# Performance work log

Hardware: AMD Instinct MI355X
Metric: run time of the kernel (lower is better)

The kernel has to match this reference:

```python
import jax, jax.numpy as jnp
import numpy as np

U, I, N, E, F, H, TOPK = 2048, 16384, 18432, 1_000_000, 64, 32, 3
NEG = -1e30  # stands in for 'structural zero' entries excluded from top-k


def setup_inputs() -> dict:
    key = jax.random.key(0)
    ks = jax.random.split(key, 6)
    x = jax.random.normal(ks[0], (N, F), dtype=jnp.float32)
    w1 = jax.random.normal(ks[1], (H, 2 * F + 2), dtype=jnp.float32) * 0.1
    b1 = jnp.zeros((H,), dtype=jnp.float32)
    w2 = jax.random.normal(ks[2], (1, H), dtype=jnp.float32) * 0.1
    b2 = jnp.zeros((1,), dtype=jnp.float32)
    edge_src = jax.random.randint(ks[3], (E,), 0, U)        # user-local == global (user_idx = arange)
    edge_dst_item = jax.random.randint(ks[4], (E,), 0, I)   # item-local; global item id = U + item
    user_idx = jnp.arange(U, dtype=jnp.int64) if jax.config.jax_enable_x64 else jnp.arange(U, dtype=jnp.int32)
    return {"x": x, "w1": w1, "b1": b1, "w2": w2, "b2": b2,
            "edge_src": edge_src, "edge_dst_item": edge_dst_item,
            "user_idx": user_idx, "num_nodes": N}


def reference(x, w1, b1, w2, b2, edge_src, edge_dst_item, user_idx, num_nodes):
    num_users = user_idx.shape[0]
    num_items = num_nodes - num_users
    u_local = edge_src           # user_idx = arange(U) so user_map is identity
    i_local = edge_dst_item      # item nodes occupy indices [U, N)

    ones = jnp.ones(u_local.shape[0], dtype=jnp.float32)
    d_u = jnp.log1p(jax.ops.segment_sum(ones, u_local, num_segments=num_users))  # [U]
    d_i = jnp.log1p(jax.ops.segment_sum(ones, i_local, num_segments=num_items))  # [I]

    # per-edge features: [u_x, log1p(deg_u), i_x, log1p(deg_i)] -> [E, 2F+2]
    x_u = x[user_idx[u_local]]
    x_it = x[num_users + i_local]
    x_e = jnp.concatenate([x_u, d_u[u_local][:, None], x_it, d_i[i_local][:, None]], axis=1)
    h = jax.nn.relu(x_e @ w1.T + b1)
    w = jax.nn.sigmoid(h @ w2.T + b2)[:, 0]  # [E], edge weights in (0,1)

    # A' [U, I] (duplicate edges coalesce-summed), C = A' A'^T with degree scaling
    A = jnp.zeros((num_users, num_items), dtype=jnp.float32).at[u_local, i_local].add(w)
    C = A @ A.T
    Dh = jnp.sqrt(d_u)
    C = C * Dh[:, None] * Dh[None, :]

    # per-row top-k restricted to structural nonzeros (all weights > 0)
    Cm = jnp.where(C > 0, C, NEG)
    vals, idx = jax.lax.top_k(Cm, TOPK)          # [U, K]
    valid = vals > 0
    vhalf = jnp.where(valid, vals, 0.0) * 0.5
    rows = jnp.broadcast_to(jnp.arange(num_users)[:, None], (num_users, TOPK))
    T = jnp.zeros((num_users, num_users), dtype=jnp.float32).at[rows, idx].add(vhalf)
    S = T + T.T  # symmetrized, deduped-by-sum adjacency; S[r,c] = val of edge (r,c)
    return S, d_u
```

## Files before the change

### kernel.cpp

```cpp
#include <hip/hip_runtime.h>
#include <hip/hip_bf16.h>
#include <math.h>

#define U_N 2048
#define I_N 16384
#define F_N 64
#define H_N 32
#define KDIM 16384
#define NEGV (-1e30f)
#define NB_DEG 256

typedef __attribute__((ext_vector_type(8))) short short8;
typedef __attribute__((ext_vector_type(4))) float f32x4;

__device__ __forceinline__ unsigned short f2bf(float f) {
    unsigned int u = __builtin_bit_cast(unsigned int, f);
    return (unsigned short)((u + 0x7fffu + ((u >> 16) & 1u)) >> 16);
}

__device__ __forceinline__ void gload16(const void* g, void* l) {
    __builtin_amdgcn_global_load_lds(
        (const __attribute__((address_space(1))) unsigned int*)g,
        (__attribute__((address_space(3))) unsigned int*)l, 16, 0, 0);
}

__global__ __launch_bounds__(256) void k_deg_part(const int* __restrict__ src,
                                                  const int* __restrict__ dst, int E,
                                                  unsigned int* __restrict__ pu,
                                                  unsigned int* __restrict__ pi2) {
    __shared__ unsigned int hu[U_N];
    __shared__ unsigned int hi2[I_N / 2];
    int tid = threadIdx.x;
    for (int t = tid; t < U_N; t += 256) hu[t] = 0u;
    for (int t = tid; t < I_N / 2; t += 256) hi2[t] = 0u;
    __syncthreads();
    const int4* s4 = (const int4*)src;
    const int4* d4 = (const int4*)dst;
    int nv = E >> 2;
    for (int v = blockIdx.x * 256 + tid; v < nv; v += NB_DEG * 256) {
        int4 u = s4[v], i = d4[v];
        atomicAdd(&hu[u.x], 1u); atomicAdd(&hi2[i.x >> 1], 1u << ((i.x & 1) * 16));
        atomicAdd(&hu[u.y], 1u); atomicAdd(&hi2[i.y >> 1], 1u << ((i.y & 1) * 16));
        atomicAdd(&hu[u.z], 1u); atomicAdd(&hi2[i.z >> 1], 1u << ((i.z & 1) * 16));
        atomicAdd(&hu[u.w], 1u); atomicAdd(&hi2[i.w >> 1], 1u << ((i.w & 1) * 16));
    }
    if (blockIdx.x == 0) {
        int e = nv * 4 + tid;
        if (e < E) {
            atomicAdd(&hu[src[e]], 1u);
            int i = dst[e];
            atomicAdd(&hi2[i >> 1], 1u << ((i & 1) * 16));
        }
    }
    __syncthreads();
    unsigned int* pub = pu + (size_t)blockIdx.x * U_N;
    unsigned int* pib = pi2 + (size_t)blockIdx.x * (I_N / 2);
    for (int t = tid; t < U_N; t += 256) pub[t] = hu[t];
    for (int t = tid; t < I_N / 2; t += 256) pib[t] = hi2[t];
}

__global__ __launch_bounds__(256) void k_node(const unsigned int* __restrict__ pu,
                                              const unsigned int* __restrict__ pi2,
                                              float* __restrict__ du,
                                              float* __restrict__ di,
                                              float* __restrict__ Dh,
                                              float* __restrict__ out_du,
                                              unsigned int* __restrict__ degu) {
    int t = blockIdx.x * 256 + threadIdx.x;
    if (t < U_N) {
        unsigned int s = 0;
        for (int b = 0; b < NB_DEG; ++b) s += pu[(size_t)b * U_N + t];
        degu[t] = s;
        float v = log1pf((float)s);
        du[t] = v;
        Dh[t] = sqrtf(v);
        out_du[t] = v;
    }
    if (t < I_N / 2) {
        unsigned int s = 0;
        for (int b = 0; b < NB_DEG; ++b) s += pi2[(size_t)b * (I_N / 2) + t];
        di[2 * t]     = log1pf((float)(s & 0xffffu));
        di[2 * t + 1] = log1pf((float)(s >> 16));
    }
}

__global__ __launch_bounds__(64) void k_scan2(const unsigned int* __restrict__ pu,
                                              const unsigned int* __restrict__ degu,
                                              unsigned int* __restrict__ base,
                                              unsigned int* __restrict__ pof) {
    __shared__ unsigned int s[U_N];
    __shared__ unsigned int csum[64];
    int tid = threadIdx.x;
    for (int t = tid; t < U_N; t += 64) s[t] = degu[t];
    __syncthreads();
    unsigned int sum = 0;
#pragma unroll
    for (int j = 0; j < 32; ++j) sum += s[tid * 32 + j];
    csum[tid] = sum;
    __syncthreads();
    if (tid == 0) {
        unsigned int run = 0;
        for (int c = 0; c < 64; ++c) { unsigned int v = csum[c]; csum[c] = run; run += v; }
    }
    __syncthreads();
    {
        unsigned int run = csum[tid];
        unsigned int ex[32];
#pragma unroll
        for (int j = 0; j < 32; ++j) { ex[j] = run; run += s[tid * 32 + j]; }
        __syncthreads();
#pragma unroll
        for (int j = 0; j < 32; ++j) s[tid * 32 + j] = ex[j];
        __syncthreads();
    }
    int u = blockIdx.x * 64 + tid;
    unsigned int run = s[u];
    base[u] = run;
    for (int b = 0; b < NB_DEG; ++b) {
        pof[(size_t)b * U_N + u] = run;
        run += pu[(size_t)b * U_N + u];
    }
}

__global__ __launch_bounds__(256) void k_esort(const int* __restrict__ src,
                                               const int* __restrict__ dst, int E,
                                               const unsigned int* __restrict__ pof,
                                               unsigned short* __restrict__ sorted) {
    __shared__ unsigned int cur[U_N];
    int tid = threadIdx.x;
    const unsigned int* p = pof + (size_t)blockIdx.x * U_N;
    for (int t = tid; t < U_N; t += 256) cur[t] = p[t];
    __syncthreads();
    const int4* s4 = (const int4*)src;
    const int4* d4 = (const int4*)dst;
    int nv = E >> 2;
    for (int v = blockIdx.x * 256 + tid; v < nv; v += NB_DEG * 256) {
        int4 u = s4[v], i = d4[v];
        sorted[atomicAdd(&cur[u.x], 1u)] = (unsigned short)i.x;
        sorted[atomicAdd(&cur[u.y], 1u)] = (unsigned short)i.y;
        sorted[atomicAdd(&cur[u.z], 1u)] = (unsigned short)i.z;
        sorted[atomicAdd(&cur[u.w], 1u)] = (unsigned short)i.w;
    }
    if (blockIdx.x == 0) {
        int e = nv * 4 + tid;
        if (e < E)
            sorted[atomicAdd(&cur[src[e]], 1u)] = (unsigned short)dst[e];
    }
}

__global__ __launch_bounds__(256) void k_proj(const float* __restrict__ x,
                                              const float* __restrict__ w1,
                                              const float* __restrict__ b1,
                                              const float* __restrict__ du,
                                              const float* __restrict__ di,
                                              float* __restrict__ Pu,
                                              float* __restrict__ Pi) {
    int t = blockIdx.x * 256 + threadIdx.x;
    if (t < U_N * H_N) {
        int u = t >> 5, j = t & 31;
        const float* xr = x + (size_t)u * F_N;
        const float* wr = w1 + (size_t)j * (2 * F_N + 2);
        float acc = b1[j] + du[u] * wr[64];
#pragma unroll
        for (int f = 0; f < F_N; ++f) acc = fmaf(xr[f], wr[f], acc);
        Pu[t] = acc;
    } else if (t < U_N * H_N + I_N * H_N) {
        int t2 = t - U_N * H_N;
        int i = t2 >> 5, j = t2 & 31;
        const float* xr = x + (size_t)(U_N + i) * F_N;
        const float* wr = w1 + (size_t)j * (2 * F_N + 2) + 65;
        float acc = di[i] * wr[64];
#pragma unroll
        for (int f = 0; f < F_N; ++f) acc = fmaf(xr[f], wr[f], acc);
        Pi[t2] = acc;
    }
}

__global__ __launch_bounds__(256) void k_edge2(const unsigned short* __restrict__ sorted,
                                               const unsigned int* __restrict__ base,
                                               const unsigned int* __restrict__ degu,
                                               const float* __restrict__ Pu,
                                               const float* __restrict__ Pi,
                                               const float* __restrict__ w2,
                                               const float* __restrict__ b2,
                                               uint4* __restrict__ Aw,
                                               float* __restrict__ diag) {
    __shared__ float hrow[I_N];
    __shared__ float red[256];
    int u = blockIdx.x, tid = threadIdx.x;
    float4* h4 = (float4*)hrow;
    float4 z4 = {0.f, 0.f, 0.f, 0.f};
#pragma unroll
    for (int j = 0; j < 16; ++j) h4[tid + j * 256] = z4;

    float pur[H_N], w2r[H_N];
#pragma unroll
    for (int j = 0; j < H_N; ++j) pur[j] = Pu[(size_t)u * H_N + j];
#pragma unroll
    for (int j = 0; j < H_N; ++j) w2r[j] = w2[j];
    float bb = b2[0];
    __syncthreads();

    int nb = (int)base[u], d = (int)degu[u];
    for (int k = tid; k < d; k += 256) {
        int i = (int)sorted[nb + k];
        const float4* pi4 = (const float4*)(Pi + (size_t)i * H_N);
        float acc = bb;
#pragma unroll
        for (int q = 0; q < H_N / 4; ++q) {
            float4 b = pi4[q];
            acc = fmaf(fmaxf(pur[4 * q + 0] + b.x, 0.f), w2r[4 * q + 0], acc);
            acc = fmaf(fmaxf(pur[4 * q + 1] + b.y, 0.f), w2r[4 * q + 1], acc);
            acc = fmaf(fmaxf(pur[4 * q + 2] + b.z, 0.f), w2r[4 * q + 2], acc);
            acc = fmaf(fmaxf(pur[4 * q + 3] + b.w, 0.f), w2r[4 * q + 3], acc);
        }
        float wgt = 1.0f / (1.0f + expf(-acc));
        atomicAdd(&hrow[i], wgt);
    }
    __syncthreads();

    uint4* row = Aw + (size_t)u * (I_N / 8);
    float ss = 0.f;
#pragma unroll
    for (int j = 0; j < 8; ++j) {
        int w = tid + j * 256;
        float4 a = h4[2 * w], b = h4[2 * w + 1];
        uint4 o;
        o.x = (unsigned int)f2bf(a.x) | ((unsigned int)f2bf(a.y) << 16);
        o.y = (unsigned int)f2bf(a.z) | ((unsigned int)f2bf(a.w) << 16);
        o.z = (unsigned int)f2bf(b.x) | ((unsigned int)f2bf(b.y) << 16);
        o.w = (unsigned int)f2bf(b.z) | ((unsigned int)f2bf(b.w) << 16);
        row[w] = o;
        ss = fmaf(a.x, a.x, ss); ss = fmaf(a.y, a.y, ss);
        ss = fmaf(a.z, a.z, ss); ss = fmaf(a.w, a.w, ss);
        ss = fmaf(b.x, b.x, ss); ss = fmaf(b.y, b.y, ss);
        ss = fmaf(b.z, b.z, ss); ss = fmaf(b.w, b.w, ss);
    }
    red[tid] = ss;
    __syncthreads();
#pragma unroll
    for (int s = 128; s > 0; s >>= 1) {
        if (tid < s) red[tid] += red[tid + s];
        __syncthreads();
    }
    if (tid == 0) diag[u] = red[0];
}

#define BM 128
#define BKS 64
#define NBLK (U_N / BM)
#define NPAIR (NBLK * (NBLK + 1) / 2)
#define KSPLIT 4
#define KCH (KDIM / KSPLIT)

__global__ __launch_bounds__(256) void k_syrk(const unsigned short* __restrict__ Abf,
                                              float* __restrict__ C) {
    __shared__ unsigned short As[BM * BKS];
    __shared__ unsigned short Bs[BM * BKS];

    int k0 = blockIdx.x * KCH;
    int p = blockIdx.y;
    int bi = 0, rem = p;
    while (rem >= NBLK - bi) { rem -= NBLK - bi; ++bi; }
    int bj = bi + rem;
    int diagp = (bi == bj);

    int tid = threadIdx.x;
    int wave = tid >> 6, lane = tid & 63;

    int srow = wave * 32 + (lane >> 3);
    int scol = ((lane & 7) ^ (lane >> 3)) * 8;
    const unsigned short* Ag = Abf + (size_t)(bi * BM + srow) * KDIM + k0 + scol;
    const unsigned short* Bg = Abf + (size_t)(bj * BM + srow) * KDIM + k0 + scol;
    unsigned short* lA = As + (wave * 32) * BKS;
    unsigned short* lB = Bs + (wave * 32) * BKS;

    int wm = wave >> 1, wn = wave & 1;
    int lm = lane & 15, lq = lane >> 4;
    int lm7 = lm & 7;
    const unsigned short* bTile = diagp ? As : Bs;

    f32x4 acc[4][4];
#pragma unroll
    for (int m = 0; m < 4; ++m)
#pragma unroll
        for (int n = 0; n < 4; ++n) acc[m][n] = (f32x4){0.f, 0.f, 0.f, 0.f};

    for (int kt = 0; kt < KCH; kt += BKS) {
        __syncthreads();
#pragma unroll
        for (int j = 0; j < 4; ++j)
            gload16(Ag + kt + (size_t)(j * 8) * KDIM, lA + j * 8 * BKS);
        if (!diagp) {
#pragma unroll
            for (int j = 0; j < 4; ++j)
                gload16(Bg + kt + (size_t)(j * 8) * KDIM, lB + j * 8 * BKS);
        }
        __syncthreads();

#pragma unroll
        for (int s = 0; s < 2; ++s) {
            int pos = ((lq + s * 4) ^ lm7) * 8;
            short8 av[4], bv[4];
#pragma unroll
            for (int m = 0; m < 4; ++m)
                av[m] = *(const short8*)(As + (wm * 64 + m * 16 + lm) * BKS + pos);
#pragma unroll
            for (int n = 0; n < 4; ++n)
                bv[n] = *(const short8*)(bTile + (wn * 64 + n * 16 + lm) * BKS + pos);
#pragma unroll
            for (int m = 0; m < 4; ++m)
#pragma unroll
                for (int n = 0; n < 4; ++n)
                    acc[m][n] = __builtin_amdgcn_mfma_f32_16x16x32_bf16(
                        av[m], bv[n], acc[m][n], 0, 0, 0);
        }
    }

#pragma unroll
    for (int m = 0; m < 4; ++m) {
        int rb = bi * BM + wm * 64 + m * 16 + lq * 4;
#pragma unroll
        for (int n = 0; n < 4; ++n) {
            int c = bj * BM + wn * 64 + n * 16 + lm;
            f32x4 v = acc[m][n];
#pragma unroll
            for (int g = 0; g < 4; ++g)
                atomicAdd(&C[(size_t)(rb + g) * U_N + c], v[g]);
        }
    }
}

__global__ __launch_bounds__(256) void k_mirror(float* __restrict__ C) {
    __shared__ float T[64][65];
    int tr = blockIdx.x, tc = blockIdx.y;
    if ((tr >> 1) <= (tc >> 1)) return;
    int lane = threadIdx.x & 63;
    int w = threadIdx.x >> 6;
#pragma unroll
    for (int s = 0; s < 16; ++s) {
        int r = s * 4 + w;
        T[r][lane] = C[(size_t)(tc * 64 + r) * U_N + tr * 64 + lane];
    }
    __syncthreads();
#pragma unroll
    for (int s = 0; s < 16; ++s) {
        int r = s * 4 + w;
        C[(size_t)(tr * 64 + r) * U_N + tc * 64 + lane] = T[lane][r];
    }
}

__device__ __forceinline__ bool better(float va, int ia, float vb, int ib) {
    return (va > vb) || (va == vb && ia < ib);
}
__device__ __forceinline__ void ins3(float v, int i, float& v0, int& i0,
                                     float& v1, int& i1, float& v2, int& i2) {
    if (better(v, i, v0, i0)) { v2 = v1; i2 = i1; v1 = v0; i1 = i0; v0 = v; i0 = i; }
    else if (better(v, i, v1, i1)) { v2 = v1; i2 = i1; v1 = v; i1 = i; }
    else if (better(v, i, v2, i2)) { v2 = v; i2 = i; }
}

__global__ __launch_bounds__(256) void k_topk(const float* __restrict__ C,
                                              const float* __restrict__ Dh,
                                              const float* __restrict__ diag,
                                              float* __restrict__ out) {
    int wave = threadIdx.x >> 6, lane = threadIdx.x & 63;
    int r = blockIdx.x * 4 + wave;
    float dr = Dh[r];
    float dex = diag[r] * dr * dr;
    float dval = (dex > 0.f) ? dex : NEGV;
    const float4* row = (const float4*)(C + (size_t)r * U_N);
    const float4* dh4 = (const float4*)Dh;
    float v0 = NEGV, v1 = NEGV, v2 = NEGV;
    int i0 = 0x7fffffff, i1 = 0x7fffffff, i2 = 0x7fffffff;
    int qr = r >> 2;
    for (int q = lane; q < U_N / 4; q += 64) {
        float4 cv = row[q];
        float4 dv = dh4[q];
        int c = q * 4;
        float x0 = (cv.x > 0.f) ? cv.x * dr * dv.x : NEGV;
        float x1 = (cv.y > 0.f) ? cv.y * dr * dv.y : NEGV;
        float x2 = (cv.z > 0.f) ? cv.z * dr * dv.z : NEGV;
        float x3 = (cv.w > 0.f) ? cv.w * dr * dv.w : NEGV;
        if (q == qr) {
            int j = r & 3;
            if (j == 0) x0 = dval; else if (j == 1) x1 = dval;
            else if (j == 2) x2 = dval; else x3 = dval;
        }
        if (better(x0, c + 0, v2, i2)) ins3(x0, c + 0, v0, i0, v1, i1, v2, i2);
        if (better(x1, c + 1, v2, i2)) ins3(x1, c + 1, v0, i0, v1, i1, v2, i2);
        if (better(x2, c + 2, v2, i2)) ins3(x2, c + 2, v0, i0, v1, i1, v2, i2);
        if (better(x3, c + 3, v2, i2)) ins3(x3, c + 3, v0, i0, v1, i1, v2, i2);
    }
#pragma unroll
    for (int off = 1; off < 64; off <<= 1) {
        float ov0 = __shfl_xor(v0, off), ov1 = __shfl_xor(v1, off), ov2 = __shfl_xor(v2, off);
        int oi0 = __shfl_xor(i0, off), oi1 = __shfl_xor(i1, off), oi2 = __shfl_xor(i2, off);
        ins3(ov0, oi0, v0, i0, v1, i1, v2, i2);
        ins3(ov1, oi1, v0, i0, v1, i1, v2, i2);
        ins3(ov2, oi2, v0, i0, v1, i1, v2, i2);
    }
    if (lane == 0) {
        float vs[3] = {v0, v1, v2};
        int is[3] = {i0, i1, i2};
#pragma unroll
        for (int k = 0; k < 3; ++k) {
            if (vs[k] > 0.f) {
                atomicAdd(&out[(size_t)r * U_N + is[k]], 0.5f * vs[k]);
                atomicAdd(&out[(size_t)is[k] * U_N + r], 0.5f * vs[k]);
            }
        }
    }
}

extern "C" void kernel_launch(void* const* d_in, const int* in_sizes, int n_in,
                              void* d_out, int out_size, void* d_ws, size_t ws_size,
                              hipStream_t stream) {
    const float* x  = (const float*)d_in[0];
    const float* w1 = (const float*)d_in[1];
    const float* b1 = (const float*)d_in[2];
    const float* w2 = (const float*)d_in[3];
    const float* b2 = (const float*)d_in[4];
    const int* esrc = (const int*)d_in[5];
    const int* edst = (const int*)d_in[6];
    int E = in_sizes[5];
    float* out = (float*)d_out;

    unsigned short* Abf = (unsigned short*)d_ws;
    float* C    = (float*)(Abf + (size_t)U_N * I_N);
    float* Pu   = C + (size_t)U_N * U_N;
    float* Pi   = Pu + (size_t)U_N * H_N;
    unsigned int* pu  = (unsigned int*)(Pi + (size_t)I_N * H_N);
    unsigned int* pi2 = pu + (size_t)NB_DEG * U_N;
    unsigned int* pof = pi2 + (size_t)NB_DEG * (I_N / 2);
    unsigned int* degu = pof + (size_t)NB_DEG * U_N;
    unsigned int* base = degu + U_N;
    float* du   = (float*)(base + U_N);
    float* di   = du + U_N;
    float* Dh   = di + I_N;
    float* diag = Dh + U_N;
    unsigned short* sorted = (unsigned short*)(diag + U_N);

    hipMemsetAsync(C, 0, (size_t)U_N * U_N * sizeof(float), stream);
    hipMemsetAsync(out, 0, (size_t)out_size * sizeof(float), stream);

    k_deg_part<<<NB_DEG, 256, 0, stream>>>(esrc, edst, E, pu, pi2);
    k_node<<<(I_N / 2 + 255) / 256, 256, 0, stream>>>(pu, pi2, du, di, Dh,
                                                      out + (size_t)U_N * U_N, degu);
    k_scan2<<<U_N / 64, 64, 0, stream>>>(pu, degu, base, pof);
    k_proj<<<(U_N * H_N + I_N * H_N) / 256, 256, 0, stream>>>(x, w1, b1, du, di, Pu, Pi);
    k_esort<<<NB_DEG, 256, 0, stream>>>(esrc, edst, E, pof, sorted);
    k_edge2<<<U_N, 256, 0, stream>>>(sorted, base, degu, Pu, Pi, w2, b2,
                                     (uint4*)Abf, diag);
    k_syrk<<<dim3(KSPLIT, NPAIR), 256, 0, stream>>>(Abf, C);
    k_mirror<<<dim3(U_N / 64, U_N / 64), 256, 0, stream>>>(C);
    k_topk<<<U_N / 4, 256, 0, stream>>>(C, Dh, diag, out);
}
```

Measured before the change: 334.5 us.

## Fuse front-end kernels into one persistent kernel with software grid barriers

```diff
diff --git a/kernel.cpp b/kernel.cpp
--- a/kernel.cpp
+++ b/kernel.cpp
@@ -8,7 +8,7 @@
 #define H_N 32
 #define KDIM 16384
 #define NEGV (-1e30f)
-#define NB_DEG 256
+#define NB 256
 
 typedef __attribute__((ext_vector_type(8))) short short8;
 typedef __attribute__((ext_vector_type(4))) float f32x4;
@@ -24,226 +24,235 @@
         (__attribute__((address_space(3))) unsigned int*)l, 16, 0, 0);
 }
 
-__global__ __launch_bounds__(256) void k_deg_part(const int* __restrict__ src,
-                                                  const int* __restrict__ dst, int E,
-                                                  unsigned int* __restrict__ pu,
-                                                  unsigned int* __restrict__ pi2) {
-    __shared__ unsigned int hu[U_N];
-    __shared__ unsigned int hi2[I_N / 2];
-    int tid = threadIdx.x;
-    for (int t = tid; t < U_N; t += 256) hu[t] = 0u;
-    for (int t = tid; t < I_N / 2; t += 256) hi2[t] = 0u;
+__device__ __forceinline__ void gridbar(unsigned int* cnt, unsigned int k) {
     __syncthreads();
-    const int4* s4 = (const int4*)src;
-    const int4* d4 = (const int4*)dst;
-    int nv = E >> 2;
-    for (int v = blockIdx.x * 256 + tid; v < nv; v += NB_DEG * 256) {
-        int4 u = s4[v], i = d4[v];
-        atomicAdd(&hu[u.x], 1u); atomicAdd(&hi2[i.x >> 1], 1u << ((i.x & 1) * 16));
-        atomicAdd(&hu[u.y], 1u); atomicAdd(&hi2[i.y >> 1], 1u << ((i.y & 1) * 16));
-        atomicAdd(&hu[u.z], 1u); atomicAdd(&hi2[i.z >> 1], 1u << ((i.z & 1) * 16));
-        atomicAdd(&hu[u.w], 1u); atomicAdd(&hi2[i.w >> 1], 1u << ((i.w & 1) * 16));
-    }
-    if (blockIdx.x == 0) {
-        int e = nv * 4 + tid;
-        if (e < E) {
-            atomicAdd(&hu[src[e]], 1u);
-            int i = dst[e];
-            atomicAdd(&hi2[i >> 1], 1u << ((i & 1) * 16));
-        }
+    if (threadIdx.x == 0) {
+        __threadfence();
+        atomicAdd(cnt, 1u);
+        while (__hip_atomic_load(cnt, __ATOMIC_RELAXED, __HIP_MEMORY_SCOPE_AGENT)
+               < k * NB)
+            __builtin_amdgcn_s_sleep(8);
+        __threadfence();
     }
     __syncthreads();
-    unsigned int* pub = pu + (size_t)blockIdx.x * U_N;
-    unsigned int* pib = pi2 + (size_t)blockIdx.x * (I_N / 2);
-    for (int t = tid; t < U_N; t += 256) pub[t] = hu[t];
-    for (int t = tid; t < I_N / 2; t += 256) pib[t] = hi2[t];
-}
-
-__global__ __launch_bounds__(256) void k_node(const unsigned int* __restrict__ pu,
-                                              const unsigned int* __restrict__ pi2,
-                                              float* __restrict__ du,
-                                              float* __restrict__ di,
-                                              float* __restrict__ Dh,
-                                              float* __restrict__ out_du,
-                                              unsigned int* __restrict__ degu) {
-    int t = blockIdx.x * 256 + threadIdx.x;
-    if (t < U_N) {
-        unsigned int s = 0;
-        for (int b = 0; b < NB_DEG; ++b) s += pu[(size_t)b * U_N + t];
-        degu[t] = s;
-        float v = log1pf((float)s);
-        du[t] = v;
-        Dh[t] = sqrtf(v);
-        out_du[t] = v;
-    }
-    if (t < I_N / 2) {
-        unsigned int s = 0;
-        for (int b = 0; b < NB_DEG; ++b) s += pi2[(size_t)b * (I_N / 2) + t];
-        di[2 * t]     = log1pf((float)(s & 0xffffu));
-        di[2 * t + 1] = log1pf((float)(s >> 16));
-    }
-}
-
-__global__ __launch_bounds__(64) void k_scan2(const unsigned int* __restrict__ pu,
-                                              const unsigned int* __restrict__ degu,
-                                              unsigned int* __restrict__ base,
-                                              unsigned int* __restrict__ pof) {
-    __shared__ unsigned int s[U_N];
-    __shared__ unsigned int csum[64];
-    int tid = threadIdx.x;
-    for (int t = tid; t < U_N; t += 64) s[t] = degu[t];
-    __syncthreads();
-    unsigned int sum = 0;
-#pragma unroll
-    for (int j = 0; j < 32; ++j) sum += s[tid * 32 + j];
-    csum[tid] = sum;
-    __syncthreads();
-    if (tid == 0) {
-        unsigned int run = 0;
-        for (int c = 0; c < 64; ++c) { unsigned int v = csum[c]; csum[c] = run; run += v; }
-    }
+}
+
+__global__ __launch_bounds__(256) void k_front(
+        const int* __restrict__ src, const int* __restrict__ dst, int E,
+        const float* __restrict__ x, const float* __restrict__ w1,
+        const float* __restrict__ b1, const float* __restrict__ w2,
+        const float* __restrict__ b2,
+        unsigned int* __restrict__ pu, unsigned int* __restrict__ pi2,
+        unsigned int* __restrict__ base, unsigned int* __restrict__ pof,
+        unsigned int* __restrict__ degu,
+        float* __restrict__ du, float* __restrict__ di, float* __restrict__ Dh,
+        float* __restrict__ diag, float* __restrict__ Pu, float* __restrict__ Pi,
+        unsigned short* __restrict__ sorted, uint4* __restrict__ Aw,
+        float* __restrict__ C, float* __restrict__ out,
+        unsigned int* __restrict__ bar) {
+    __shared__ union {
+        struct { unsigned int hu[U_N]; unsigned int hi2[I_N / 2]; } h;
+        struct { unsigned int s[U_N]; unsigned int csum[256]; } sc;
+        unsigned int cur[U_N];
+        struct { float hrow[I_N]; float red[4]; } e;
+    } sm;
+
+    int bid = blockIdx.x, tid = threadIdx.x;
+    const float4 z4 = {0.f, 0.f, 0.f, 0.f};
+
+    for (int t = tid; t < U_N; t += 256) sm.h.hu[t] = 0u;
+    for (int t = tid; t < I_N / 2; t += 256) sm.h.hi2[t] = 0u;
     __syncthreads();
     {
-        unsigned int run = csum[tid];
-        unsigned int ex[32];
-#pragma unroll
-        for (int j = 0; j < 32; ++j) { ex[j] = run; run += s[tid * 32 + j]; }
-        __syncthreads();
-#pragma unroll
-        for (int j = 0; j < 32; ++j) s[tid * 32 + j] = ex[j];
-        __syncthreads();
-    }
-    int u = blockIdx.x * 64 + tid;
-    unsigned int run = s[u];
-    base[u] = run;
-    for (int b = 0; b < NB_DEG; ++b) {
-        pof[(size_t)b * U_N + u] = run;
-        run += pu[(size_t)b * U_N + u];
-    }
-}
-
-__global__ __launch_bounds__(256) void k_esort(const int* __restrict__ src,
-                                               const int* __restrict__ dst, int E,
-                                               const unsigned int* __restrict__ pof,
-                                               unsigned short* __restrict__ sorted) {
-    __shared__ unsigned int cur[U_N];
-    int tid = threadIdx.x;
-    const unsigned int* p = pof + (size_t)blockIdx.x * U_N;
-    for (int t = tid; t < U_N; t += 256) cur[t] = p[t];
+        const int4* s4 = (const int4*)src;
+        const int4* d4 = (const int4*)dst;
+        int nv = E >> 2;
+        for (int v = bid * 256 + tid; v < nv; v += NB * 256) {
+            int4 u = s4[v], i = d4[v];
+            atomicAdd(&sm.h.hu[u.x], 1u); atomicAdd(&sm.h.hi2[i.x >> 1], 1u << ((i.x & 1) * 16));
+            atomicAdd(&sm.h.hu[u.y], 1u); atomicAdd(&sm.h.hi2[i.y >> 1], 1u << ((i.y & 1) * 16));
+            atomicAdd(&sm.h.hu[u.z], 1u); atomicAdd(&sm.h.hi2[i.z >> 1], 1u << ((i.z & 1) * 16));
+            atomicAdd(&sm.h.hu[u.w], 1u); atomicAdd(&sm.h.hi2[i.w >> 1], 1u << ((i.w & 1) * 16));
+        }
+        if (bid == 0) {
+            int e = nv * 4 + tid;
+            if (e < E) {
+                atomicAdd(&sm.h.hu[src[e]], 1u);
+                int i = dst[e];
+                atomicAdd(&sm.h.hi2[i >> 1], 1u << ((i & 1) * 16));
+            }
+        }
+    }
     __syncthreads();
-    const int4* s4 = (const int4*)src;
-    const int4* d4 = (const int4*)dst;
-    int nv = E >> 2;
-    for (int v = blockIdx.x * 256 + tid; v < nv; v += NB_DEG * 256) {
-        int4 u = s4[v], i = d4[v];
-        sorted[atomicAdd(&cur[u.x], 1u)] = (unsigned short)i.x;
-        sorted[atomicAdd(&cur[u.y], 1u)] = (unsigned short)i.y;
-        sorted[atomicAdd(&cur[u.z], 1u)] = (unsigned short)i.z;
-        sorted[atomicAdd(&cur[u.w], 1u)] = (unsigned short)i.w;
-    }
-    if (blockIdx.x == 0) {
-        int e = nv * 4 + tid;
-        if (e < E)
-            sorted[atomicAdd(&cur[src[e]], 1u)] = (unsigned short)dst[e];
-    }
-}
-
-__global__ __launch_bounds__(256) void k_proj(const float* __restrict__ x,
-                                              const float* __restrict__ w1,
-                                              const float* __restrict__ b1,
-                                              const float* __restrict__ du,
-                                              const float* __restrict__ di,
-                                              float* __restrict__ Pu,
-                                              float* __restrict__ Pi) {
-    int t = blockIdx.x * 256 + threadIdx.x;
-    if (t < U_N * H_N) {
-        int u = t >> 5, j = t & 31;
-        const float* xr = x + (size_t)u * F_N;
-        const float* wr = w1 + (size_t)j * (2 * F_N + 2);
-        float acc = b1[j] + du[u] * wr[64];
-#pragma unroll
-        for (int f = 0; f < F_N; ++f) acc = fmaf(xr[f], wr[f], acc);
-        Pu[t] = acc;
-    } else if (t < U_N * H_N + I_N * H_N) {
-        int t2 = t - U_N * H_N;
-        int i = t2 >> 5, j = t2 & 31;
-        const float* xr = x + (size_t)(U_N + i) * F_N;
-        const float* wr = w1 + (size_t)j * (2 * F_N + 2) + 65;
-        float acc = di[i] * wr[64];
-#pragma unroll
-        for (int f = 0; f < F_N; ++f) acc = fmaf(xr[f], wr[f], acc);
-        Pi[t2] = acc;
-    }
-}
-
-__global__ __launch_bounds__(256) void k_edge2(const unsigned short* __restrict__ sorted,
-                                               const unsigned int* __restrict__ base,
-                                               const unsigned int* __restrict__ degu,
-                                               const float* __restrict__ Pu,
-                                               const float* __restrict__ Pi,
-                                               const float* __restrict__ w2,
-                                               const float* __restrict__ b2,
-                                               uint4* __restrict__ Aw,
-                                               float* __restrict__ diag) {
-    __shared__ float hrow[I_N];
-    __shared__ float red[256];
-    int u = blockIdx.x, tid = threadIdx.x;
-    float4* h4 = (float4*)hrow;
-    float4 z4 = {0.f, 0.f, 0.f, 0.f};
-#pragma unroll
-    for (int j = 0; j < 16; ++j) h4[tid + j * 256] = z4;
-
-    float pur[H_N], w2r[H_N];
-#pragma unroll
-    for (int j = 0; j < H_N; ++j) pur[j] = Pu[(size_t)u * H_N + j];
-#pragma unroll
-    for (int j = 0; j < H_N; ++j) w2r[j] = w2[j];
-    float bb = b2[0];
-    __syncthreads();
-
-    int nb = (int)base[u], d = (int)degu[u];
-    for (int k = tid; k < d; k += 256) {
-        int i = (int)sorted[nb + k];
-        const float4* pi4 = (const float4*)(Pi + (size_t)i * H_N);
-        float acc = bb;
-#pragma unroll
-        for (int q = 0; q < H_N / 4; ++q) {
-            float4 b = pi4[q];
-            acc = fmaf(fmaxf(pur[4 * q + 0] + b.x, 0.f), w2r[4 * q + 0], acc);
-            acc = fmaf(fmaxf(pur[4 * q + 1] + b.y, 0.f), w2r[4 * q + 1], acc);
-            acc = fmaf(fmaxf(pur[4 * q + 2] + b.z, 0.f), w2r[4 * q + 2], acc);
-            acc = fmaf(fmaxf(pur[4 * q + 3] + b.w, 0.f), w2r[4 * q + 3], acc);
-        }
-        float wgt = 1.0f / (1.0f + expf(-acc));
-        atomicAdd(&hrow[i], wgt);
-    }
-    __syncthreads();
-
-    uint4* row = Aw + (size_t)u * (I_N / 8);
-    float ss = 0.f;
-#pragma unroll
-    for (int j = 0; j < 8; ++j) {
-        int w = tid + j * 256;
-        float4 a = h4[2 * w], b = h4[2 * w + 1];
-        uint4 o;
-        o.x = (unsigned int)f2bf(a.x) | ((unsigned int)f2bf(a.y) << 16);
-        o.y = (unsigned int)f2bf(a.z) | ((unsigned int)f2bf(a.w) << 16);
-        o.z = (unsigned int)f2bf(b.x) | ((unsigned int)f2bf(b.y) << 16);
-        o.w = (unsigned int)f2bf(b.z) | ((unsigned int)f2bf(b.w) << 16);
-        row[w] = o;
-        ss = fmaf(a.x, a.x, ss); ss = fmaf(a.y, a.y, ss);
-        ss = fmaf(a.z, a.z, ss); ss = fmaf(a.w, a.w, ss);
-        ss = fmaf(b.x, b.x, ss); ss = fmaf(b.y, b.y, ss);
-        ss = fmaf(b.z, b.z, ss); ss = fmaf(b.w, b.w, ss);
-    }
-    red[tid] = ss;
-    __syncthreads();
-#pragma unroll
-    for (int s = 128; s > 0; s >>= 1) {
-        if (tid < s) red[tid] += red[tid + s];
-        __syncthreads();
-    }
-    if (tid == 0) diag[u] = red[0];
+    {
+        unsigned int* pub = pu + (size_t)bid * U_N;
+        unsigned int* pib = pi2 + (size_t)bid * (I_N / 2);
+        for (int t = tid; t < U_N; t += 256) pub[t] = sm.h.hu[t];
+        for (int t = tid; t < I_N / 2; t += 256) pib[t] = sm.h.hi2[t];
+        float4* C4 = (float4*)C;
+        for (int t = bid * 256 + tid; t < U_N * U_N / 4; t += NB * 256) C4[t] = z4;
+        float4* o4 = (float4*)out;
+        for (int t = bid * 256 + tid; t < (U_N * U_N + U_N) / 4; t += NB * 256) o4[t] = z4;
+    }
+    gridbar(bar, 1);
+
+    {
+        int t = bid * 256 + tid;
+        if (t < U_N) {
+            unsigned int s = 0;
+            for (int b = 0; b < NB; ++b) s += pu[(size_t)b * U_N + t];
+            degu[t] = s;
+            float v = log1pf((float)s);
+            du[t] = v;
+            Dh[t] = sqrtf(v);
+            out[(size_t)U_N * U_N + t] = v;
+        }
+        if (t < I_N / 2) {
+            unsigned int s = 0;
+            for (int b = 0; b < NB; ++b) s += pi2[(size_t)b * (I_N / 2) + t];
+            di[2 * t]     = log1pf((float)(s & 0xffffu));
+            di[2 * t + 1] = log1pf((float)(s >> 16));
+        }
+    }
+    gridbar(bar, 2);
+
+    if (bid < 8) {
+        for (int t = tid; t < U_N; t += 256) sm.sc.s[t] = degu[t];
+        __syncthreads();
+        unsigned int sum = 0;
+#pragma unroll
+        for (int j = 0; j < 8; ++j) sum += sm.sc.s[tid * 8 + j];
+        sm.sc.csum[tid] = sum;
+        __syncthreads();
+        if (tid == 0) {
+            unsigned int run = 0;
+            for (int c = 0; c < 256; ++c) {
+                unsigned int v = sm.sc.csum[c]; sm.sc.csum[c] = run; run += v;
+            }
+        }
+        __syncthreads();
+        {
+            unsigned int run = sm.sc.csum[tid];
+            unsigned int ex[8];
+#pragma unroll
+            for (int j = 0; j < 8; ++j) { ex[j] = run; run += sm.sc.s[tid * 8 + j]; }
+            __syncthreads();
+#pragma unroll
+            for (int j = 0; j < 8; ++j) sm.sc.s[tid * 8 + j] = ex[j];
+            __syncthreads();
+        }
+        int u = bid * 256 + tid;
+        unsigned int run = sm.sc.s[u];
+        base[u] = run;
+        for (int b = 0; b < NB; ++b) {
+            pof[(size_t)b * U_N + u] = run;
+            run += pu[(size_t)b * U_N + u];
+        }
+    } else {
+        const int NP = (U_N + I_N) * H_N;
+        for (int t = (bid - 8) * 256 + tid; t < NP; t += (NB - 8) * 256) {
+            if (t < U_N * H_N) {
+                int u = t >> 5, j = t & 31;
+                const float* xr = x + (size_t)u * F_N;
+                const float* wr = w1 + (size_t)j * (2 * F_N + 2);
+                float acc = b1[j] + du[u] * wr[64];
+#pragma unroll
+                for (int f = 0; f < F_N; ++f) acc = fmaf(xr[f], wr[f], acc);
+                Pu[t] = acc;
+            } else {
+                int t2 = t - U_N * H_N;
+                int i = t2 >> 5, j = t2 & 31;
+                const float* xr = x + (size_t)(U_N + i) * F_N;
+                const float* wr = w1 + (size_t)j * (2 * F_N + 2) + 65;
+                float acc = di[i] * wr[64];
+#pragma unroll
+                for (int f = 0; f < F_N; ++f) acc = fmaf(xr[f], wr[f], acc);
+                Pi[t2] = acc;
+            }
+        }
+    }
+    gridbar(bar, 3);
+
+    {
+        const unsigned int* p = pof + (size_t)bid * U_N;
+        for (int t = tid; t < U_N; t += 256) sm.cur[t] = p[t];
+        __syncthreads();
+        const int4* s4 = (const int4*)src;
+        const int4* d4 = (const int4*)dst;
+        int nv = E >> 2;
+        for (int v = bid * 256 + tid; v < nv; v += NB * 256) {
+            int4 u = s4[v], i = d4[v];
+            sorted[atomicAdd(&sm.cur[u.x], 1u)] = (unsigned short)i.x;
+            sorted[atomicAdd(&sm.cur[u.y], 1u)] = (unsigned short)i.y;
+            sorted[atomicAdd(&sm.cur[u.z], 1u)] = (unsigned short)i.z;
+            sorted[atomicAdd(&sm.cur[u.w], 1u)] = (unsigned short)i.w;
+        }
+        if (bid == 0) {
+            int e = nv * 4 + tid;
+            if (e < E)
+                sorted[atomicAdd(&sm.cur[src[e]], 1u)] = (unsigned short)dst[e];
+        }
+    }
+    gridbar(bar, 4);
+
+    {
+        float w2r[H_N];
+#pragma unroll
+        for (int j = 0; j < H_N; ++j) w2r[j] = w2[j];
+        float bb = b2[0];
+        int wave = tid >> 6, lane = tid & 63;
+        float4* h4 = (float4*)sm.e.hrow;
+        for (int uu = 0; uu < 8; ++uu) {
+            int u = bid * 8 + uu;
+#pragma unroll
+            for (int j = 0; j < 16; ++j) h4[tid + j * 256] = z4;
+            float pur[H_N];
+#pragma unroll
+            for (int j = 0; j < H_N; ++j) pur[j] = Pu[(size_t)u * H_N + j];
+            __syncthreads();
+            int nb0 = (int)base[u], d = (int)degu[u];
+            for (int k = tid; k < d; k += 256) {
+                int i = (int)sorted[nb0 + k];
+                const float4* pi4 = (const float4*)(Pi + (size_t)i * H_N);
+                float acc = bb;
+#pragma unroll
+                for (int q = 0; q < H_N / 4; ++q) {
+                    float4 b = pi4[q];
+                    acc = fmaf(fmaxf(pur[4 * q + 0] + b.x, 0.f), w2r[4 * q + 0], acc);
+                    acc = fmaf(fmaxf(pur[4 * q + 1] + b.y, 0.f), w2r[4 * q + 1], acc);
+                    acc = fmaf(fmaxf(pur[4 * q + 2] + b.z, 0.f), w2r[4 * q + 2], acc);
+                    acc = fmaf(fmaxf(pur[4 * q + 3] + b.w, 0.f), w2r[4 * q + 3], acc);
+                }
+                float wgt = 1.0f / (1.0f + expf(-acc));
+                atomicAdd(&sm.e.hrow[i], wgt);
+            }
+            __syncthreads();
+            uint4* row = Aw + (size_t)u * (I_N / 8);
+            float ss = 0.f;
+#pragma unroll
+            for (int j = 0; j < 8; ++j) {
+                int w = tid + j * 256;
+                float4 a = h4[2 * w], b = h4[2 * w + 1];
+                uint4 o;
+                o.x = (unsigned int)f2bf(a.x) | ((unsigned int)f2bf(a.y) << 16);
+                o.y = (unsigned int)f2bf(a.z) | ((unsigned int)f2bf(a.w) << 16);
+                o.z = (unsigned int)f2bf(b.x) | ((unsigned int)f2bf(b.y) << 16);
+                o.w = (unsigned int)f2bf(b.z) | ((unsigned int)f2bf(b.w) << 16);
+                row[w] = o;
+                ss = fmaf(a.x, a.x, ss); ss = fmaf(a.y, a.y, ss);
+                ss = fmaf(a.z, a.z, ss); ss = fmaf(a.w, a.w, ss);
+                ss = fmaf(b.x, b.x, ss); ss = fmaf(b.y, b.y, ss);
+                ss = fmaf(b.z, b.z, ss); ss = fmaf(b.w, b.w, ss);
+            }
+#pragma unroll
+            for (int off = 32; off > 0; off >>= 1) ss += __shfl_down(ss, off);
+            if (lane == 0) sm.e.red[wave] = ss;
+            __syncthreads();
+            if (tid == 0)
+                diag[u] = sm.e.red[0] + sm.e.red[1] + sm.e.red[2] + sm.e.red[3];
+            __syncthreads();
+        }
+    }
 }
 
 #define BM 128
@@ -431,27 +440,22 @@
     float* Pu   = C + (size_t)U_N * U_N;
     float* Pi   = Pu + (size_t)U_N * H_N;
     unsigned int* pu  = (unsigned int*)(Pi + (size_t)I_N * H_N);
-    unsigned int* pi2 = pu + (size_t)NB_DEG * U_N;
-    unsigned int* pof = pi2 + (size_t)NB_DEG * (I_N / 2);
-    unsigned int* degu = pof + (size_t)NB_DEG * U_N;
+    unsigned int* pi2 = pu + (size_t)NB * U_N;
+    unsigned int* pof = pi2 + (size_t)NB * (I_N / 2);
+    unsigned int* degu = pof + (size_t)NB * U_N;
     unsigned int* base = degu + U_N;
     float* du   = (float*)(base + U_N);
     float* di   = du + U_N;
     float* Dh   = di + I_N;
     float* diag = Dh + U_N;
     unsigned short* sorted = (unsigned short*)(diag + U_N);
-
-    hipMemsetAsync(C, 0, (size_t)U_N * U_N * sizeof(float), stream);
-    hipMemsetAsync(out, 0, (size_t)out_size * sizeof(float), stream);
-
-    k_deg_part<<<NB_DEG, 256, 0, stream>>>(esrc, edst, E, pu, pi2);
-    k_node<<<(I_N / 2 + 255) / 256, 256, 0, stream>>>(pu, pi2, du, di, Dh,
-                                                      out + (size_t)U_N * U_N, degu);
-    k_scan2<<<U_N / 64, 64, 0, stream>>>(pu, degu, base, pof);
-    k_proj<<<(U_N * H_N + I_N * H_N) / 256, 256, 0, stream>>>(x, w1, b1, du, di, Pu, Pi);
-    k_esort<<<NB_DEG, 256, 0, stream>>>(esrc, edst, E, pof, sorted);
-    k_edge2<<<U_N, 256, 0, stream>>>(sorted, base, degu, Pu, Pi, w2, b2,
-                                     (uint4*)Abf, diag);
+    unsigned int* bar = (unsigned int*)(sorted + ((E + 7) & ~7));
+
+    hipMemsetAsync(bar, 0, sizeof(unsigned int), stream);
+
+    k_front<<<NB, 256, 0, stream>>>(esrc, edst, E, x, w1, b1, w2, b2,
+                                    pu, pi2, base, pof, degu, du, di, Dh, diag,
+                                    Pu, Pi, sorted, (uint4*)Abf, C, out, bar);
     k_syrk<<<dim3(KSPLIT, NPAIR), 256, 0, stream>>>(Abf, C);
     k_mirror<<<dim3(U_N / 64, U_N / 64), 256, 0, stream>>>(C);
     k_topk<<<U_N / 4, 256, 0, stream>>>(C, Dh, diag, out);
```

Result: slower. 409.8 us (+22.5%).

## Fold memsets into degree kernel and parallelize degree reduction and offset scan

Applied to the files above, without the earlier changes.

```diff
diff --git a/kernel.cpp b/kernel.cpp
--- a/kernel.cpp
+++ b/kernel.cpp
@@ -27,7 +27,9 @@
 __global__ __launch_bounds__(256) void k_deg_part(const int* __restrict__ src,
                                                   const int* __restrict__ dst, int E,
                                                   unsigned int* __restrict__ pu,
-                                                  unsigned int* __restrict__ pi2) {
+                                                  unsigned int* __restrict__ pi2,
+                                                  float* __restrict__ C,
+                                                  float* __restrict__ out) {
     __shared__ unsigned int hu[U_N];
     __shared__ unsigned int hi2[I_N / 2];
     int tid = threadIdx.x;
@@ -57,68 +59,108 @@
     unsigned int* pib = pi2 + (size_t)blockIdx.x * (I_N / 2);
     for (int t = tid; t < U_N; t += 256) pub[t] = hu[t];
     for (int t = tid; t < I_N / 2; t += 256) pib[t] = hi2[t];
-}
-
-__global__ __launch_bounds__(256) void k_node(const unsigned int* __restrict__ pu,
-                                              const unsigned int* __restrict__ pi2,
-                                              float* __restrict__ du,
-                                              float* __restrict__ di,
-                                              float* __restrict__ Dh,
-                                              float* __restrict__ out_du,
-                                              unsigned int* __restrict__ degu) {
-    int t = blockIdx.x * 256 + threadIdx.x;
-    if (t < U_N) {
-        unsigned int s = 0;
-        for (int b = 0; b < NB_DEG; ++b) s += pu[(size_t)b * U_N + t];
-        degu[t] = s;
-        float v = log1pf((float)s);
-        du[t] = v;
-        Dh[t] = sqrtf(v);
-        out_du[t] = v;
-    }
-    if (t < I_N / 2) {
-        unsigned int s = 0;
-        for (int b = 0; b < NB_DEG; ++b) s += pi2[(size_t)b * (I_N / 2) + t];
-        di[2 * t]     = log1pf((float)(s & 0xffffu));
-        di[2 * t + 1] = log1pf((float)(s >> 16));
-    }
-}
-
-__global__ __launch_bounds__(64) void k_scan2(const unsigned int* __restrict__ pu,
-                                              const unsigned int* __restrict__ degu,
-                                              unsigned int* __restrict__ base,
-                                              unsigned int* __restrict__ pof) {
-    __shared__ unsigned int s[U_N];
-    __shared__ unsigned int csum[64];
+    const float4 z4 = {0.f, 0.f, 0.f, 0.f};
+    float4* C4 = (float4*)C;
+    for (int t = blockIdx.x * 256 + tid; t < U_N * U_N / 4; t += NB_DEG * 256)
+        C4[t] = z4;
+    float4* o4 = (float4*)out;
+    for (int t = blockIdx.x * 256 + tid; t < (U_N * U_N + U_N) / 4; t += NB_DEG * 256)
+        o4[t] = z4;
+}
+
+__global__ __launch_bounds__(256) void k_node2(const unsigned int* __restrict__ pu,
+                                               const unsigned int* __restrict__ pi2,
+                                               float* __restrict__ du,
+                                               float* __restrict__ di,
+                                               float* __restrict__ Dh,
+                                               float* __restrict__ out_du,
+                                               unsigned int* __restrict__ degu) {
+    __shared__ unsigned int red[8][32];
+    int j = threadIdx.x >> 5, l = threadIdx.x & 31;
+    int e = blockIdx.x * 32 + l;
+    unsigned int s = 0;
+    if (e < U_N) {
+        const unsigned int* p = pu + e;
+#pragma unroll
+        for (int k = 0; k < 32; ++k) s += p[(size_t)(j * 32 + k) * U_N];
+    } else {
+        const unsigned int* p = pi2 + (e - U_N);
+#pragma unroll
+        for (int k = 0; k < 32; ++k) s += p[(size_t)(j * 32 + k) * (I_N / 2)];
+    }
+    red[j][l] = s;
+    __syncthreads();
+    if (threadIdx.x < 32) {
+        unsigned int t = 0;
+#pragma unroll
+        for (int jj = 0; jj < 8; ++jj) t += red[jj][l];
+        if (e < U_N) {
+            degu[e] = t;
+            float v = log1pf((float)t);
+            du[e] = v;
+            Dh[e] = sqrtf(v);
+            out_du[e] = v;
+        } else {
+            int ii = e - U_N;
+            di[2 * ii]     = log1pf((float)(t & 0xffffu));
+            di[2 * ii + 1] = log1pf((float)(t >> 16));
+        }
+    }
+}
+
+__global__ __launch_bounds__(256) void k_pof(const unsigned int* __restrict__ pu,
+                                             const unsigned int* __restrict__ degu,
+                                             unsigned int* __restrict__ base,
+                                             unsigned int* __restrict__ pof) {
+    __shared__ unsigned int dg[U_N];
+    __shared__ unsigned int wt[4];
+    __shared__ unsigned int ps[8][32];
     int tid = threadIdx.x;
-    for (int t = tid; t < U_N; t += 64) s[t] = degu[t];
-    __syncthreads();
+    int wave = tid >> 6, lane = tid & 63;
+    for (int t = tid; t < U_N; t += 256) dg[t] = degu[t];
+    __syncthreads();
+    unsigned int loc[8];
+    unsigned int s = 0;
+#pragma unroll
+    for (int j = 0; j < 8; ++j) { loc[j] = dg[tid * 8 + j]; s += loc[j]; }
+    unsigned int inc = s;
+#pragma unroll
+    for (int off = 1; off < 64; off <<= 1) {
+        unsigned int o = __shfl_up(inc, off);
+        if (lane >= off) inc += o;
+    }
+    if (lane == 63) wt[wave] = inc;
+    __syncthreads();
+    unsigned int woff = 0;
+#pragma unroll
+    for (int w = 0; w < 4; ++w) woff += (w < wave) ? wt[w] : 0u;
+    unsigned int ex = woff + inc - s;
+    __syncthreads();
+    {
+        unsigned int run = ex;
+#pragma unroll
+        for (int j = 0; j < 8; ++j) { unsigned int v = loc[j]; dg[tid * 8 + j] = run; run += v; }
+    }
+    __syncthreads();
+    int c = tid >> 5, l = tid & 31;
+    int u = blockIdx.x * 32 + l;
+    if (c == 0) base[u] = dg[u];
+    unsigned int v32[32];
     unsigned int sum = 0;
 #pragma unroll
-    for (int j = 0; j < 32; ++j) sum += s[tid * 32 + j];
-    csum[tid] = sum;
-    __syncthreads();
-    if (tid == 0) {
-        unsigned int run = 0;
-        for (int c = 0; c < 64; ++c) { unsigned int v = csum[c]; csum[c] = run; run += v; }
-    }
-    __syncthreads();
-    {
-        unsigned int run = csum[tid];
-        unsigned int ex[32];
-#pragma unroll
-        for (int j = 0; j < 32; ++j) { ex[j] = run; run += s[tid * 32 + j]; }
-        __syncthreads();
-#pragma unroll
-        for (int j = 0; j < 32; ++j) s[tid * 32 + j] = ex[j];
-        __syncthreads();
-    }
-    int u = blockIdx.x * 64 + tid;
-    unsigned int run = s[u];
-    base[u] = run;
-    for (int b = 0; b < NB_DEG; ++b) {
-        pof[(size_t)b * U_N + u] = run;
-        run += pu[(size_t)b * U_N + u];
+    for (int k = 0; k < 32; ++k) {
+        v32[k] = pu[(size_t)(c * 32 + k) * U_N + u];
+        sum += v32[k];
+    }
+    ps[c][l] = sum;
+    __syncthreads();
+    unsigned int run = dg[u];
+#pragma unroll
+    for (int c2 = 0; c2 < 8; ++c2) run += (c2 < c) ? ps[c2][l] : 0u;
+#pragma unroll
+    for (int k = 0; k < 32; ++k) {
+        pof[(size_t)(c * 32 + k) * U_N + u] = run;
+        run += v32[k];
     }
 }
 
@@ -441,13 +483,10 @@
     float* diag = Dh + U_N;
     unsigned short* sorted = (unsigned short*)(diag + U_N);
 
-    hipMemsetAsync(C, 0, (size_t)U_N * U_N * sizeof(float), stream);
-    hipMemsetAsync(out, 0, (size_t)out_size * sizeof(float), stream);
-
-    k_deg_part<<<NB_DEG, 256, 0, stream>>>(esrc, edst, E, pu, pi2);
-    k_node<<<(I_N / 2 + 255) / 256, 256, 0, stream>>>(pu, pi2, du, di, Dh,
+    k_deg_part<<<NB_DEG, 256, 0, stream>>>(esrc, edst, E, pu, pi2, C, out);
+    k_node2<<<(U_N + I_N / 2) / 32, 256, 0, stream>>>(pu, pi2, du, di, Dh,
                                                       out + (size_t)U_N * U_N, degu);
-    k_scan2<<<U_N / 64, 64, 0, stream>>>(pu, degu, base, pof);
+    k_pof<<<U_N / 32, 256, 0, stream>>>(pu, degu, base, pof);
     k_proj<<<(U_N * H_N + I_N * H_N) / 256, 256, 0, stream>>>(x, w1, b1, du, di, Pu, Pi);
     k_esort<<<NB_DEG, 256, 0, stream>>>(esrc, edst, E, pof, sorted);
     k_edge2<<<U_N, 256, 0, stream>>>(sorted, base, degu, Pu, Pi, w2, b2,
```

Result: faster. 299.9 us (-10.3%).
